# Performance work log

Measured on AMD Instinct MI355X. Metric: run time of the kernel, lower is better.

The kernel has to match this reference:

```python
import jax, jax.numpy as jnp
import numpy as np

B, S, H, KVH, D, HID = 2, 2048, 32, 8, 128, 4096
WINDOW = 512
EPS = 1e-5
SCALE = D ** -0.5
NEG = jnp.finfo(jnp.float32).min


def cohere_layernorm(x, w):
    # true LayerNorm (mean-subtracting), fp32 compute, weight, no bias
    xf = x.astype(jnp.float32)
    mu = jnp.mean(xf, axis=-1, keepdims=True)
    var = jnp.mean((xf - mu) ** 2, axis=-1, keepdims=True)
    return (w.astype(jnp.float32) * (xf - mu) * jax.lax.rsqrt(var + EPS)).astype(x.dtype)


def rotate_half_interleaved(x):
    # interleaved pairs: (x0,x1,x2,x3,...) -> (-x1,x0,-x3,x2,...)
    x1 = x[..., ::2]
    x2 = x[..., 1::2]
    return jnp.stack([-x2, x1], axis=-1).reshape(x.shape)


def setup_inputs() -> dict:
    key = jax.random.key(0)
    ks = jax.random.split(key, 6)
    hidden_states = jax.random.normal(ks[0], (B, S, HID), jnp.float32)
    position_ids = jnp.broadcast_to(jnp.arange(S, dtype=jnp.int32), (B, S))
    # rotary table with interleave-repeated frequencies (Cohere style)
    inv_freq = 1.0 / (10000.0 ** (jnp.arange(0, D, 2, dtype=jnp.float32) / D))
    freqs = jnp.arange(S, dtype=jnp.float32)[:, None] * inv_freq[None, :]  # [S, D/2]
    emb = jnp.repeat(freqs, 2, axis=-1)  # [S, D]
    cos, sin = jnp.cos(emb), jnp.sin(emb)
    std = 0.02
    # weights stored [in, out] so projection is x @ W
    wq = jax.random.normal(ks[1], (HID, H * D), jnp.float32) * std
    wk = jax.random.normal(ks[2], (HID, KVH * D), jnp.float32) * std
    wv = jax.random.normal(ks[3], (HID, KVH * D), jnp.float32) * std
    wo = jax.random.normal(ks[4], (H * D, HID), jnp.float32) * std
    q_norm_w = jnp.ones((D,), jnp.float32)
    k_norm_w = jnp.ones((D,), jnp.float32)
    return {"hidden_states": hidden_states, "position_ids": position_ids,
            "cos": cos, "sin": sin, "wq": wq, "wk": wk, "wv": wv, "wo": wo,
            "q_norm_w": q_norm_w, "k_norm_w": k_norm_w}


def reference(hidden_states, position_ids, cos, sin, wq, wk, wv, wo, q_norm_w, k_norm_w):
    q = (hidden_states @ wq).reshape(B, S, H, D)
    k = (hidden_states @ wk).reshape(B, S, KVH, D)
    v = (hidden_states @ wv).reshape(B, S, KVH, D)
    # QK LayerNorm over head_dim
    q = cohere_layernorm(q, q_norm_w)
    k = cohere_layernorm(k, k_norm_w)
    # interleaved RoPE; cos/sin gathered by position then broadcast over heads (unsqueeze_dim=2)
    c = cos[position_ids][:, :, None, :]  # [B, S, 1, D]
    s = sin[position_ids][:, :, None, :]
    q = q * c + rotate_half_interleaved(q) * s
    k = k * c + rotate_half_interleaved(k) * s
    # GQA: expand KV heads, attention in bhsd layout
    rep = H // KVH
    qh = jnp.transpose(q, (0, 2, 1, 3))                      # [B, H, S, D]
    kh = jnp.transpose(jnp.repeat(k, rep, axis=2), (0, 2, 1, 3))
    vh = jnp.transpose(jnp.repeat(v, rep, axis=2), (0, 2, 1, 3))
    scores = jnp.einsum('bhqd,bhkd->bhqk', qh, kh) * SCALE   # [B, H, S, S]
    i = jnp.arange(S)[:, None]
    j = jnp.arange(S)[None, :]
    mask = (i >= j) & (i - j < WINDOW)                       # causal + sliding window
    scores = jnp.where(mask[None, None], scores, NEG)
    attn = jax.nn.softmax(scores, axis=-1)
    out = jnp.einsum('bhqk,bhkd->bhqd', attn, vh)
    out = jnp.transpose(out, (0, 2, 1, 3)).reshape(B, S, H * D)
    return out @ wo
```

## Files before the change

kernel.cpp:

```cpp
#include <hip/hip_runtime.h>
#include <hip/hip_bf16.h>
#include <cstdio>
#include <cstdint>

#define B_    2
#define S_    2048
#define H_    32
#define KVH_  8
#define D_    128
#define HID_  4096
#define WIN_  512
#define NROW_ (B_*S_)
#define NKV_  2048
#define SCALE_ 0.08838834764831845f
#define SL2E_  0.12751744932973953f

typedef __attribute__((ext_vector_type(8))) __bf16 bf16x8;
typedef __attribute__((ext_vector_type(4))) __bf16 bf16x4;
typedef __attribute__((ext_vector_type(4))) float  f32x4;

#define GAS __attribute__((address_space(1)))
#define LAS __attribute__((address_space(3)))

__global__ __launch_bounds__(256) void cvt_bf16(const float* __restrict__ in,
                                                __hip_bfloat16* __restrict__ out, int n) {
    int i = (blockIdx.x * 256 + threadIdx.x) * 4;
    if (i >= n) return;
    float4 v = *(const float4*)(in + i);
    __hip_bfloat162 a, b;
    a.x = __float2bfloat16(v.x); a.y = __float2bfloat16(v.y);
    b.x = __float2bfloat16(v.z); b.y = __float2bfloat16(v.w);
    *(__hip_bfloat162*)(out + i)     = a;
    *(__hip_bfloat162*)(out + i + 2) = b;
}

__global__ __launch_bounds__(256) void transpose_cvt(const float* __restrict__ in,
                                                     __hip_bfloat16* __restrict__ out,
                                                     int R, int C) {
    __shared__ float t[32][33];
    int tx = threadIdx.x, ty = threadIdx.y;
    int r0 = blockIdx.y * 32, c0 = blockIdx.x * 32;
    #pragma unroll
    for (int i = 0; i < 4; ++i)
        t[ty + 8*i][tx] = in[(size_t)(r0 + ty + 8*i) * C + c0 + tx];
    __syncthreads();
    #pragma unroll
    for (int i = 0; i < 4; ++i)
        out[(size_t)(c0 + ty + 8*i) * R + r0 + tx] = __float2bfloat16(t[tx][ty + 8*i]);
}

__global__ __launch_bounds__(256) void v_transpose(const float* __restrict__ kvf,
                                                   __hip_bfloat16* __restrict__ vt) {
    __shared__ float t[32][33];
    int tx = threadIdx.x, ty = threadIdx.y;
    int plane = blockIdx.z, b = plane >> 3, g = plane & 7;
    int s0 = blockIdx.x * 32, d0 = blockIdx.y * 32;
    #pragma unroll
    for (int i = 0; i < 4; ++i) {
        int s = s0 + ty + 8*i;
        t[ty + 8*i][tx] = kvf[((size_t)b*S_ + s) * NKV_ + (KVH_*D_) + g*D_ + d0 + tx];
    }
    __syncthreads();
    #pragma unroll
    for (int i = 0; i < 4; ++i) {
        int d = d0 + ty + 8*i;
        vt[(((size_t)b*KVH_ + g) * D_ + d) * S_ + s0 + tx] = __float2bfloat16(t[tx][ty + 8*i]);
    }
}

template <int FN>
__global__ __launch_bounds__(512, 2) void gemm_t(const __hip_bfloat16* __restrict__ A,
                                                 const __hip_bfloat16* __restrict__ Bt,
                                                 float* __restrict__ C,
                                                 int M, int N, int K, int nbx) {
    constexpr int BN   = FN * 64;
    constexpr int BLD  = BN / 128;
    constexpr int SLOT = (256 + BN) * 32;
    __shared__ __align__(16) __hip_bfloat16 L[4 * SLOT];
    const int tid  = threadIdx.x;
    const int lane = tid & 63, w = tid >> 6;
    const int wm = w >> 2, wn = w & 3;
    const int lc = lane & 15, lg = lane >> 4;
    const int nwg = gridDim.x, cpx = nwg >> 3;
    const int bid = blockIdx.x;
    const int swz = (bid & 7) * cpx + (bid >> 3);
    const int by = swz / nbx, bx = swz - by * nbx;
    const size_t row0 = (size_t)by * 256, col0 = (size_t)bx * BN;
    const int nt = K >> 5;

    const int srow = tid >> 2;
    const int spc  = tid & 3;
    const int slx  = spc ^ ((srow >> 1) & 3);
    const __hip_bfloat16* Ab = A  + row0 * K;
    const __hip_bfloat16* Bb = Bt + col0 * K;

#define STGA(tile_) do {                                                                   \
    const int ss_ = (tile_) & 3;                                                           \
    const int kt_ = ((tile_) < nt) ? (tile_) : (nt - 1);  \
    _Pragma("unroll")                                                                      \
    for (int rh_ = 0; rh_ < 2; ++rh_)                                                      \
        __builtin_amdgcn_global_load_lds(                                                  \
            (const GAS void*)(Ab + (size_t)(rh_*128 + srow) * K + kt_*32 + slx*8),         \
            (LAS void*)&L[ss_*SLOT + rh_*4096 + w*512], 16, 0, 0);                         \
} while (0)

#define STGB(tile_) do {                                                                   \
    const int ss_ = (tile_) & 3;                                                           \
    const int kt_ = ((tile_) < nt) ? (tile_) : (nt - 1);                                   \
    _Pragma("unroll")                                                                      \
    for (int bh_ = 0; bh_ < BLD; ++bh_)                                                    \
        __builtin_amdgcn_global_load_lds(                                                  \
            (const GAS void*)(Bb + (size_t)(bh_*128 + srow) * K + kt_*32 + slx*8),         \
            (LAS void*)&L[ss_*SLOT + 8192 + bh_*4096 + w*512], 16, 0, 0);                  \
} while (0)

    f32x4 acc[2][4][FN] = {};
    bf16x8 afr[4], bfr[FN];

    STGA(0); STGB(0); STGA(1); STGB(1); STGA(2); STGB(2);
    if constexpr (FN == 4) asm volatile("s_waitcnt vmcnt(8)" ::: "memory");
    else                   asm volatile("s_waitcnt vmcnt(6)" ::: "memory");
    asm volatile("s_barrier" ::: "memory");

    for (int t = 0; t < nt; ++t) {
        const int s_ = t & 3;

        #pragma unroll
        for (int fn = 0; fn < FN; ++fn) {
            const int rB = wn*(FN*16) + fn*16 + lc;
            bfr[fn] = *(const bf16x8*)&L[s_*SLOT + 8192 + rB*32 + ((lg ^ ((rB >> 1) & 3)) * 8)];
        }
        #pragma unroll
        for (int fm = 0; fm < 4; ++fm) {
            const int rA = wm*128 + fm*16 + lc;
            afr[fm] = *(const bf16x8*)&L[s_*SLOT + rA*32 + ((lg ^ ((rA >> 1) & 3)) * 8)];
        }
        STGA(t + 3);
        if constexpr (FN == 4) asm volatile("s_waitcnt vmcnt(10)" ::: "memory");
        else                   asm volatile("s_waitcnt vmcnt(8)"  ::: "memory");
        asm volatile("s_barrier" ::: "memory");
        asm volatile("s_waitcnt lgkmcnt(0)" ::: "memory");
        __builtin_amdgcn_sched_barrier(0);
        __builtin_amdgcn_s_setprio(1);
        #pragma unroll
        for (int fm = 0; fm < 4; ++fm)
            #pragma unroll
            for (int fn = 0; fn < FN; ++fn)
                acc[0][fm][fn] = __builtin_amdgcn_mfma_f32_16x16x32_bf16(
                    afr[fm], bfr[fn], acc[0][fm][fn], 0, 0, 0);
        __builtin_amdgcn_s_setprio(0);

        #pragma unroll
        for (int fm = 0; fm < 4; ++fm) {
            const int rA = wm*128 + 64 + fm*16 + lc;
            afr[fm] = *(const bf16x8*)&L[s_*SLOT + rA*32 + ((lg ^ ((rA >> 1) & 3)) * 8)];
        }
        STGB(t + 3);
        asm volatile("s_waitcnt lgkmcnt(0)" ::: "memory");
        __builtin_amdgcn_sched_barrier(0);
        __builtin_amdgcn_s_setprio(1);
        #pragma unroll
        for (int fm = 0; fm < 4; ++fm)
            #pragma unroll
            for (int fn = 0; fn < FN; ++fn)
                acc[1][fm][fn] = __builtin_amdgcn_mfma_f32_16x16x32_bf16(
                    afr[fm], bfr[fn], acc[1][fm][fn], 0, 0, 0);
        __builtin_amdgcn_s_setprio(0);
        asm volatile("s_barrier" ::: "memory");
    }
#undef STGA
#undef STGB
    asm volatile("s_waitcnt vmcnt(0)" ::: "memory");

    #pragma unroll
    for (int qm = 0; qm < 2; ++qm)
        #pragma unroll
        for (int fm = 0; fm < 4; ++fm)
            #pragma unroll
            for (int fn = 0; fn < FN; ++fn) {
                const size_t col = col0 + wn*(FN*16) + fn*16 + lc;
                #pragma unroll
                for (int rr = 0; rr < 4; ++rr) {
                    const size_t row = row0 + wm*128 + qm*64 + fm*16 + lg*4 + rr;
                    C[row * N + col] = acc[qm][fm][fn][rr];
                }
            }
}

template <int NH, int LD, int XOFF>
__global__ __launch_bounds__(256) void ln_rope(const float* __restrict__ x,
                                               const float* __restrict__ wln,
                                               const float* __restrict__ cosT,
                                               const float* __restrict__ sinT,
                                               const int* __restrict__ pids,
                                               __hip_bfloat16* __restrict__ out) {
    const int lane = threadIdx.x & 63, wv = threadIdx.x >> 6;
    const int r = blockIdx.x * 4 + wv;
    const int h = r % NH;
    const int bs = r / NH;
    const int b = bs / S_, s = bs % S_;
    const float2 xv = *(const float2*)(x + (size_t)bs * LD + XOFF + h*D_ + lane*2);
    float sum = xv.x + xv.y;
    #pragma unroll
    for (int o = 32; o; o >>= 1) sum += __shfl_xor(sum, o);
    const float mu = sum * (1.f / D_);
    const float dx = xv.x - mu, dy = xv.y - mu;
    float vs = dx*dx + dy*dy;
    #pragma unroll
    for (int o = 32; o; o >>= 1) vs += __shfl_xor(vs, o);
    const float rs = rsqrtf(vs * (1.f / D_) + 1e-5f);
    const float2 w2 = *(const float2*)(wln + lane*2);
    const float y0 = w2.x * dx * rs, y1 = w2.y * dy * rs;
    const int p = pids[bs];
    const float2 c  = *(const float2*)(cosT + (size_t)p * D_ + lane*2);
    const float2 sn = *(const float2*)(sinT + (size_t)p * D_ + lane*2);
    __hip_bfloat162 ov;
    ov.x = __float2bfloat16(y0 * c.x - y1 * sn.x);
    ov.y = __float2bfloat16(y1 * c.y + y0 * sn.y);
    *(__hip_bfloat162*)(out + (((size_t)b * NH + h) * S_ + s) * D_ + lane*2) = ov;
}

static __device__ __forceinline__ int sigk_(int r) { return (r & 3) | ((r >> 1) & 4); }

__global__ __launch_bounds__(256) void attn_fwd(const __hip_bfloat16* __restrict__ qr,
                                                const __hip_bfloat16* __restrict__ kr,
                                                const __hip_bfloat16* __restrict__ vt,
                                                __hip_bfloat16* __restrict__ ao) {
    __shared__ __align__(16) __hip_bfloat16 Ksl[2][64*D_];
    __shared__ __align__(16) __hip_bfloat16 Vsl[2][D_*64];
    const int lane = threadIdx.x & 63, w = threadIdx.x >> 6;
    const int lq = lane & 15, lg = lane >> 4;
    const int blk = blockIdx.x;
    const int qt = blk >> 6;
    const int bh = blk & 63;
    const int h = bh & (H_-1), b = bh >> 5;
    const int g = h >> 2;
    const int q0 = qt*64 + w*16;
    const int q  = q0 + lq;

    const __hip_bfloat16* qbase = qr + (((size_t)b*H_ + h)*S_ + q0) * D_;
    const __hip_bfloat16* kbase = kr + ((size_t)b*KVH_ + g) * (size_t)S_ * D_;
    const __hip_bfloat16* vbase = vt + ((size_t)b*KVH_ + g) * (size_t)D_ * S_;

    const int srK = lane >> 4, scK = lane & 15;
    const int srV = lane >> 3, scV = lane & 7;

#define STAGE(nb, k0s) do {                                                              \
    _Pragma("unroll")                                                                    \
    for (int s_ = 0; s_ < 4; ++s_) {                                                     \
        const int rK_ = s_*16 + w*4 + srK;                                               \
        const __hip_bfloat16* srcK_ = kbase + (size_t)((k0s) + rK_)*D_                   \
                                      + ((scK ^ sigk_(rK_)) * 8);                        \
        __builtin_amdgcn_global_load_lds((const GAS void*)srcK_,                         \
            (LAS void*)&Ksl[nb][(s_*16 + w*4)*D_], 16, 0, 0);                            \
    }                                                                                    \
    _Pragma("unroll")                                                                    \
    for (int s_ = 0; s_ < 4; ++s_) {                                                     \
        const int dV_ = s_*32 + w*8 + srV;                                               \
        const __hip_bfloat16* srcV_ = vbase + (size_t)dV_*S_ + (k0s)                     \
                                      + ((scV ^ (dV_ & 7)) * 8);                         \
        __builtin_amdgcn_global_load_lds((const GAS void*)srcV_,                         \
            (LAS void*)&Vsl[nb][(s_*32 + w*8)*64], 16, 0, 0);                            \
    }                                                                                    \
} while (0)

    bf16x8 qf[4];
    #pragma unroll
    for (int kk = 0; kk < 4; ++kk)
        qf[kk] = *(const bf16x8*)(qbase + lq*D_ + kk*32 + lg*8);

    f32x4 o[8] = {};
    float m = -1e30f, l = 0.f;

    int kst = qt*64 - (WIN_ - 1); if (kst < 0) kst = 0; kst &= ~63;
    const int nt = qt + 1 - (kst >> 6);
    const int kldrow = 8*(lq >> 2) + (lq & 3);

    STAGE(0, kst);

    for (int t = 0; t < nt; ++t) {
        const int k0 = kst + t*64;
        const int buf = t & 1;
        if (t + 1 < nt) {
            STAGE((t + 1) & 1, k0 + 64);
            asm volatile("s_waitcnt vmcnt(8)" ::: "memory");
        } else {
            asm volatile("s_waitcnt vmcnt(0)" ::: "memory");
        }
        __builtin_amdgcn_s_barrier();

        f32x4 sc[2][2] = {};
        __builtin_amdgcn_s_setprio(1);
        #pragma unroll
        for (int kb = 0; kb < 2; ++kb)
            #pragma unroll
            for (int f = 0; f < 2; ++f) {
                const int rA = kb*32 + 4*f + kldrow;
                const __hip_bfloat16* kp = &Ksl[buf][rA*D_];
                #pragma unroll
                for (int kk = 0; kk < 4; ++kk) {
                    bf16x8 ka = *(const bf16x8*)(kp + (((kk*4 + lg) ^ sigk_(rA)) * 8));
                    sc[kb][f] = __builtin_amdgcn_mfma_f32_16x16x32_bf16(ka, qf[kk], sc[kb][f], 0, 0, 0);
                }
            }
        __builtin_amdgcn_s_setprio(0);

        const int dqk = q - (k0 + 8*lg);
        float pv[16];
        float mx = -INFINITY;
        #pragma unroll
        for (int kb = 0; kb < 2; ++kb)
            #pragma unroll
            for (int f = 0; f < 2; ++f)
                #pragma unroll
                for (int r = 0; r < 4; ++r) {
                    const int c = kb*32 + 4*f + r;
                    const int d = dqk - c;
                    float v = (d >= 0 && d < WIN_) ? sc[kb][f][r] * SL2E_ : -INFINITY;
                    pv[kb*8 + f*4 + r] = v;
                    mx = fmaxf(mx, v);
                }
        mx = fmaxf(mx, __shfl_xor(mx, 16));
        mx = fmaxf(mx, __shfl_xor(mx, 32));
        const float mn = fmaxf(m, mx);
        const float alpha = exp2f(m - mn);
        float ls = 0.f;
        union { bf16x8 v; __hip_bfloat16 e[8]; } pu[2];
        #pragma unroll
        for (int kb = 0; kb < 2; ++kb)
            #pragma unroll
            for (int j = 0; j < 8; ++j) {
                const float p = exp2f(pv[kb*8 + j] - mn);
                ls += p;
                pu[kb].e[j] = __float2bfloat16(p);
            }
        ls += __shfl_xor(ls, 16);
        ls += __shfl_xor(ls, 32);
        l = l * alpha + ls;
        m = mn;
        #pragma unroll
        for (int n = 0; n < 8; ++n) {
            o[n][0] *= alpha; o[n][1] *= alpha; o[n][2] *= alpha; o[n][3] *= alpha;
        }

        __builtin_amdgcn_s_setprio(1);
        #pragma unroll
        for (int kb = 0; kb < 2; ++kb)
            #pragma unroll
            for (int n = 0; n < 8; ++n) {
                const int dR = n*16 + lq;
                bf16x8 vf8 = *(const bf16x8*)(&Vsl[buf][dR*64] + (((kb*4 + lg) ^ (dR & 7)) * 8));
                o[n] = __builtin_amdgcn_mfma_f32_16x16x32_bf16(vf8, pu[kb].v, o[n], 0, 0, 0);
            }
        __builtin_amdgcn_s_setprio(0);

        if (t + 1 < nt) __builtin_amdgcn_s_barrier();
    }
#undef STAGE

    const float rinv = 1.f / l;
    #pragma unroll
    for (int n = 0; n < 8; ++n) {
        union { bf16x4 v; __hip_bfloat16 e[4]; } ov;
        #pragma unroll
        for (int r = 0; r < 4; ++r) ov.e[r] = __float2bfloat16(o[n][r] * rinv);
        *(bf16x4*)(ao + ((size_t)b*S_ + q)*(H_*D_) + h*D_ + n*16 + lg*4) = ov.v;
    }
}

extern "C" void kernel_launch(void* const* d_in, const int* in_sizes, int n_in,
                              void* d_out, int out_size, void* d_ws, size_t ws_size,
                              hipStream_t stream) {
    const float* hidden = (const float*)d_in[0];
    const int*   pids   = (const int*)  d_in[1];
    const float* cosT   = (const float*)d_in[2];
    const float* sinT   = (const float*)d_in[3];
    const float* wq     = (const float*)d_in[4];
    const float* wk     = (const float*)d_in[5];
    const float* wv     = (const float*)d_in[6];
    const float* wo     = (const float*)d_in[7];
    const float* qnw    = (const float*)d_in[8];
    const float* knw    = (const float*)d_in[9];
    float* out = (float*)d_out;

    char* base = (char*)d_ws;
    size_t off = 0;
    auto take = [&](size_t bytes) -> void* {
        void* q = base + off;
        off = (off + bytes + 255) & ~(size_t)255;
        return q;
    };
    float* qf            = (float*)take((size_t)NROW_*HID_*4);
    float* kvf           = (float*)take((size_t)NROW_*NKV_*4);
    __hip_bfloat16* hb   = (__hip_bfloat16*)take((size_t)NROW_*HID_*2);
    __hip_bfloat16* wqT  = (__hip_bfloat16*)take((size_t)HID_*HID_*2);
    __hip_bfloat16* wkvT = (__hip_bfloat16*)take((size_t)NKV_*HID_*2);
    __hip_bfloat16* woT  = (__hip_bfloat16*)take((size_t)HID_*HID_*2);
    __hip_bfloat16* qr   = (__hip_bfloat16*)take((size_t)B_*H_*S_*D_*2);
    __hip_bfloat16* kr   = (__hip_bfloat16*)take((size_t)B_*KVH_*S_*D_*2);
    __hip_bfloat16* vt   = (__hip_bfloat16*)take((size_t)B_*KVH_*S_*D_*2);
    __hip_bfloat16* ao   = (__hip_bfloat16*)qf;

    if (off > ws_size) {
        fprintf(stderr, "WORKSPACE TOO SMALL: need %zu have %zu\n", off, ws_size);
        return;
    }

    cvt_bf16<<<(NROW_*HID_)/1024, 256, 0, stream>>>(hidden, hb, NROW_*HID_);
    transpose_cvt<<<dim3((H_*D_)/32,   HID_/32), dim3(32,8), 0, stream>>>(wq, wqT, HID_, H_*D_);
    transpose_cvt<<<dim3((KVH_*D_)/32, HID_/32), dim3(32,8), 0, stream>>>(wk, wkvT, HID_, KVH_*D_);
    transpose_cvt<<<dim3((KVH_*D_)/32, HID_/32), dim3(32,8), 0, stream>>>(wv, wkvT + (size_t)(KVH_*D_)*HID_, HID_, KVH_*D_);
    transpose_cvt<<<dim3(HID_/32, (H_*D_)/32),   dim3(32,8), 0, stream>>>(wo, woT, H_*D_, HID_);

    gemm_t<4><<<(NROW_/256)*(HID_/256), 512, 0, stream>>>(hb, wqT,  qf,  NROW_, HID_, HID_, HID_/256);
    gemm_t<2><<<(NROW_/256)*(NKV_/128), 512, 0, stream>>>(hb, wkvT, kvf, NROW_, NKV_, HID_, NKV_/128);

    ln_rope<H_,   HID_, 0><<<(B_*S_*H_)/4,   256, 0, stream>>>(qf,  qnw, cosT, sinT, pids, qr);
    ln_rope<KVH_, NKV_, 0><<<(B_*S_*KVH_)/4, 256, 0, stream>>>(kvf, knw, cosT, sinT, pids, kr);
    v_transpose<<<dim3(S_/32, D_/32, B_*KVH_), dim3(32,8), 0, stream>>>(kvf, vt);

    attn_fwd<<<B_*H_*(S_/64), 256, 0, stream>>>(qr, kr, vt, ao);

    gemm_t<4><<<(NROW_/256)*(HID_/256), 512, 0, stream>>>(ao, woT, out, NROW_, HID_, H_*D_, HID_/256);
}
```

Measured before the change: 513.2 us.

## Fuse V transpose into KV GEMM epilogue, emit bf16 projections, merge weight transposes

```diff
diff --git a/kernel.cpp b/kernel.cpp
--- a/kernel.cpp
+++ b/kernel.cpp
@@ -34,47 +34,40 @@
     *(__hip_bfloat162*)(out + i + 2) = b;
 }
 
-__global__ __launch_bounds__(256) void transpose_cvt(const float* __restrict__ in,
-                                                     __hip_bfloat16* __restrict__ out,
-                                                     int R, int C) {
+__global__ __launch_bounds__(256) void wtrans_all(const float* __restrict__ wq,
+                                                  const float* __restrict__ wk,
+                                                  const float* __restrict__ wv,
+                                                  const float* __restrict__ wo,
+                                                  __hip_bfloat16* __restrict__ wqT,
+                                                  __hip_bfloat16* __restrict__ wkvT,
+                                                  __hip_bfloat16* __restrict__ woT) {
     __shared__ float t[32][33];
-    int tx = threadIdx.x, ty = threadIdx.y;
-    int r0 = blockIdx.y * 32, c0 = blockIdx.x * 32;
+    const int tx = threadIdx.x, ty = threadIdx.y;
+    const int bid = blockIdx.x;
+    const float* src; __hip_bfloat16* dst; int C, idx;
+    if (bid < 16384)      { src = wq; dst = wqT;  C = 4096; idx = bid; }
+    else if (bid < 20480) { src = wk; dst = wkvT; C = 1024; idx = bid - 16384; }
+    else if (bid < 24576) { src = wv; dst = wkvT + (size_t)1024*HID_; C = 1024; idx = bid - 20480; }
+    else                  { src = wo; dst = woT;  C = 4096; idx = bid - 24576; }
+    const int ctiles = C >> 5;
+    const int c0 = (idx % ctiles) * 32, r0 = (idx / ctiles) * 32;
     #pragma unroll
     for (int i = 0; i < 4; ++i)
-        t[ty + 8*i][tx] = in[(size_t)(r0 + ty + 8*i) * C + c0 + tx];
+        t[ty + 8*i][tx] = src[(size_t)(r0 + ty + 8*i) * C + c0 + tx];
     __syncthreads();
     #pragma unroll
     for (int i = 0; i < 4; ++i)
-        out[(size_t)(c0 + ty + 8*i) * R + r0 + tx] = __float2bfloat16(t[tx][ty + 8*i]);
-}
-
-__global__ __launch_bounds__(256) void v_transpose(const float* __restrict__ kvf,
-                                                   __hip_bfloat16* __restrict__ vt) {
-    __shared__ float t[32][33];
-    int tx = threadIdx.x, ty = threadIdx.y;
-    int plane = blockIdx.z, b = plane >> 3, g = plane & 7;
-    int s0 = blockIdx.x * 32, d0 = blockIdx.y * 32;
-    #pragma unroll
-    for (int i = 0; i < 4; ++i) {
-        int s = s0 + ty + 8*i;
-        t[ty + 8*i][tx] = kvf[((size_t)b*S_ + s) * NKV_ + (KVH_*D_) + g*D_ + d0 + tx];
-    }
-    __syncthreads();
-    #pragma unroll
-    for (int i = 0; i < 4; ++i) {
-        int d = d0 + ty + 8*i;
-        vt[(((size_t)b*KVH_ + g) * D_ + d) * S_ + s0 + tx] = __float2bfloat16(t[tx][ty + 8*i]);
-    }
-}
-
-template <int FN>
+        dst[(size_t)(c0 + ty + 8*i) * HID_ + r0 + tx] = __float2bfloat16(t[tx][ty + 8*i]);
+}
+
+template <int FN, int OMODE>
 __global__ __launch_bounds__(512, 2) void gemm_t(const __hip_bfloat16* __restrict__ A,
                                                  const __hip_bfloat16* __restrict__ Bt,
-                                                 float* __restrict__ C,
+                                                 void* __restrict__ Cv, void* __restrict__ C2,
                                                  int M, int N, int K, int nbx) {
     constexpr int BN   = FN * 64;
     constexpr int BLD  = BN / 128;
+    constexpr int LPT  = 2 + BLD;
     constexpr int SLOT = (256 + BN) * 32;
     __shared__ __align__(16) __hip_bfloat16 L[4 * SLOT];
     const int tid  = threadIdx.x;
@@ -114,12 +107,16 @@
             (LAS void*)&L[ss_*SLOT + 8192 + bh_*4096 + w*512], 16, 0, 0);                  \
 } while (0)
 
+#define VMW2L() do {                                                                       \
+    if constexpr (FN == 4) asm volatile("s_waitcnt vmcnt(8)" ::: "memory");                \
+    else                   asm volatile("s_waitcnt vmcnt(6)" ::: "memory");                \
+} while (0)
+
     f32x4 acc[2][4][FN] = {};
     bf16x8 afr[4], bfr[FN];
 
     STGA(0); STGB(0); STGA(1); STGB(1); STGA(2); STGB(2);
-    if constexpr (FN == 4) asm volatile("s_waitcnt vmcnt(8)" ::: "memory");
-    else                   asm volatile("s_waitcnt vmcnt(6)" ::: "memory");
+    VMW2L();
     asm volatile("s_barrier" ::: "memory");
 
     for (int t = 0; t < nt; ++t) {
@@ -136,8 +133,6 @@
             afr[fm] = *(const bf16x8*)&L[s_*SLOT + rA*32 + ((lg ^ ((rA >> 1) & 3)) * 8)];
         }
         STGA(t + 3);
-        if constexpr (FN == 4) asm volatile("s_waitcnt vmcnt(10)" ::: "memory");
-        else                   asm volatile("s_waitcnt vmcnt(8)"  ::: "memory");
         asm volatile("s_barrier" ::: "memory");
         asm volatile("s_waitcnt lgkmcnt(0)" ::: "memory");
         __builtin_amdgcn_sched_barrier(0);
@@ -166,29 +161,92 @@
                 acc[1][fm][fn] = __builtin_amdgcn_mfma_f32_16x16x32_bf16(
                     afr[fm], bfr[fn], acc[1][fm][fn], 0, 0, 0);
         __builtin_amdgcn_s_setprio(0);
+        VMW2L();
         asm volatile("s_barrier" ::: "memory");
     }
 #undef STGA
 #undef STGB
+#undef VMW2L
     asm volatile("s_waitcnt vmcnt(0)" ::: "memory");
 
-    #pragma unroll
-    for (int qm = 0; qm < 2; ++qm)
-        #pragma unroll
-        for (int fm = 0; fm < 4; ++fm)
-            #pragma unroll
-            for (int fn = 0; fn < FN; ++fn) {
-                const size_t col = col0 + wn*(FN*16) + fn*16 + lc;
-                #pragma unroll
-                for (int rr = 0; rr < 4; ++rr) {
-                    const size_t row = row0 + wm*128 + qm*64 + fm*16 + lg*4 + rr;
-                    C[row * N + col] = acc[qm][fm][fn][rr];
+    if constexpr (OMODE == 0) {
+        float* C = (float*)Cv;
+        #pragma unroll
+        for (int qm = 0; qm < 2; ++qm)
+            #pragma unroll
+            for (int fm = 0; fm < 4; ++fm)
+                #pragma unroll
+                for (int fn = 0; fn < FN; ++fn) {
+                    const size_t col = col0 + wn*(FN*16) + fn*16 + lc;
+                    #pragma unroll
+                    for (int rr = 0; rr < 4; ++rr) {
+                        const size_t row = row0 + wm*128 + qm*64 + fm*16 + lg*4 + rr;
+                        C[row * N + col] = acc[qm][fm][fn][rr];
+                    }
                 }
+    } else if constexpr (OMODE == 1) {
+        __hip_bfloat16* C = (__hip_bfloat16*)Cv;
+        #pragma unroll
+        for (int qm = 0; qm < 2; ++qm)
+            #pragma unroll
+            for (int fm = 0; fm < 4; ++fm)
+                #pragma unroll
+                for (int fn = 0; fn < FN; ++fn) {
+                    const size_t col = col0 + wn*(FN*16) + fn*16 + lc;
+                    #pragma unroll
+                    for (int rr = 0; rr < 4; ++rr) {
+                        const size_t row = row0 + wm*128 + qm*64 + fm*16 + lg*4 + rr;
+                        C[row * N + col] = __float2bfloat16(acc[qm][fm][fn][rr]);
+                    }
+                }
+    } else {
+        if (bx < 8) {
+            __hip_bfloat16* C = (__hip_bfloat16*)Cv;
+            #pragma unroll
+            for (int qm = 0; qm < 2; ++qm)
+                #pragma unroll
+                for (int fm = 0; fm < 4; ++fm)
+                    #pragma unroll
+                    for (int fn = 0; fn < FN; ++fn) {
+                        const size_t col = col0 + wn*32 + fn*16 + lc;
+                        #pragma unroll
+                        for (int rr = 0; rr < 4; ++rr) {
+                            const size_t row = row0 + wm*128 + qm*64 + fm*16 + lg*4 + rr;
+                            C[row * 1024 + col] = __float2bfloat16(acc[qm][fm][fn][rr]);
+                        }
+                    }
+        } else {
+            __hip_bfloat16* lt = (__hip_bfloat16*)L;
+            __syncthreads();
+            #pragma unroll
+            for (int qm = 0; qm < 2; ++qm)
+                #pragma unroll
+                for (int fm = 0; fm < 4; ++fm)
+                    #pragma unroll
+                    for (int fn = 0; fn < FN; ++fn) {
+                        const int cl = wn*32 + fn*16 + lc;
+                        #pragma unroll
+                        for (int rr = 0; rr < 4; ++rr) {
+                            const int rl = wm*128 + qm*64 + fm*16 + lg*4 + rr;
+                            lt[cl*264 + rl] = __float2bfloat16(acc[qm][fm][fn][rr]);
+                        }
+                    }
+            __syncthreads();
+            const int bb = (int)(row0 >> 11), s0 = (int)(row0 & 2047);
+            const int g  = (int)((col0 - 1024) >> 7);
+            __hip_bfloat16* vto = (__hip_bfloat16*)C2 + (((size_t)bb*KVH_ + g) * D_) * (size_t)S_;
+            const int d = tid >> 2, sc0 = (tid & 3) * 64;
+            #pragma unroll
+            for (int j = 0; j < 64; j += 8) {
+                bf16x8 v = *(const bf16x8*)&lt[d*264 + sc0 + j];
+                *(bf16x8*)&vto[(size_t)d*S_ + s0 + sc0 + j] = v;
             }
+        }
+    }
 }
 
 template <int NH, int LD, int XOFF>
-__global__ __launch_bounds__(256) void ln_rope(const float* __restrict__ x,
+__global__ __launch_bounds__(256) void ln_rope(const __hip_bfloat16* __restrict__ x,
                                                const float* __restrict__ wln,
                                                const float* __restrict__ cosT,
                                                const float* __restrict__ sinT,
@@ -199,12 +257,13 @@
     const int h = r % NH;
     const int bs = r / NH;
     const int b = bs / S_, s = bs % S_;
-    const float2 xv = *(const float2*)(x + (size_t)bs * LD + XOFF + h*D_ + lane*2);
-    float sum = xv.x + xv.y;
+    const __hip_bfloat162 xv2 = *(const __hip_bfloat162*)(x + (size_t)bs * LD + XOFF + h*D_ + lane*2);
+    const float x0 = __bfloat162float(xv2.x), x1 = __bfloat162float(xv2.y);
+    float sum = x0 + x1;
     #pragma unroll
     for (int o = 32; o; o >>= 1) sum += __shfl_xor(sum, o);
     const float mu = sum * (1.f / D_);
-    const float dx = xv.x - mu, dy = xv.y - mu;
+    const float dx = x0 - mu, dy = x1 - mu;
     float vs = dx*dx + dy*dy;
     #pragma unroll
     for (int o = 32; o; o >>= 1) vs += __shfl_xor(vs, o);
@@ -390,8 +449,8 @@
         off = (off + bytes + 255) & ~(size_t)255;
         return q;
     };
-    float* qf            = (float*)take((size_t)NROW_*HID_*4);
-    float* kvf           = (float*)take((size_t)NROW_*NKV_*4);
+    __hip_bfloat16* qfb  = (__hip_bfloat16*)take((size_t)NROW_*HID_*2);
+    __hip_bfloat16* kf   = (__hip_bfloat16*)take((size_t)NROW_*1024*2);
     __hip_bfloat16* hb   = (__hip_bfloat16*)take((size_t)NROW_*HID_*2);
     __hip_bfloat16* wqT  = (__hip_bfloat16*)take((size_t)HID_*HID_*2);
     __hip_bfloat16* wkvT = (__hip_bfloat16*)take((size_t)NKV_*HID_*2);
@@ -399,7 +458,7 @@
     __hip_bfloat16* qr   = (__hip_bfloat16*)take((size_t)B_*H_*S_*D_*2);
     __hip_bfloat16* kr   = (__hip_bfloat16*)take((size_t)B_*KVH_*S_*D_*2);
     __hip_bfloat16* vt   = (__hip_bfloat16*)take((size_t)B_*KVH_*S_*D_*2);
-    __hip_bfloat16* ao   = (__hip_bfloat16*)qf;
+    __hip_bfloat16* ao   = qfb;
 
     if (off > ws_size) {
         fprintf(stderr, "WORKSPACE TOO SMALL: need %zu have %zu\n", off, ws_size);
@@ -407,19 +466,15 @@
     }
 
     cvt_bf16<<<(NROW_*HID_)/1024, 256, 0, stream>>>(hidden, hb, NROW_*HID_);
-    transpose_cvt<<<dim3((H_*D_)/32,   HID_/32), dim3(32,8), 0, stream>>>(wq, wqT, HID_, H_*D_);
-    transpose_cvt<<<dim3((KVH_*D_)/32, HID_/32), dim3(32,8), 0, stream>>>(wk, wkvT, HID_, KVH_*D_);
-    transpose_cvt<<<dim3((KVH_*D_)/32, HID_/32), dim3(32,8), 0, stream>>>(wv, wkvT + (size_t)(KVH_*D_)*HID_, HID_, KVH_*D_);
-    transpose_cvt<<<dim3(HID_/32, (H_*D_)/32),   dim3(32,8), 0, stream>>>(wo, woT, H_*D_, HID_);
-
-    gemm_t<4><<<(NROW_/256)*(HID_/256), 512, 0, stream>>>(hb, wqT,  qf,  NROW_, HID_, HID_, HID_/256);
-    gemm_t<2><<<(NROW_/256)*(NKV_/128), 512, 0, stream>>>(hb, wkvT, kvf, NROW_, NKV_, HID_, NKV_/128);
-
-    ln_rope<H_,   HID_, 0><<<(B_*S_*H_)/4,   256, 0, stream>>>(qf,  qnw, cosT, sinT, pids, qr);
-    ln_rope<KVH_, NKV_, 0><<<(B_*S_*KVH_)/4, 256, 0, stream>>>(kvf, knw, cosT, sinT, pids, kr);
-    v_transpose<<<dim3(S_/32, D_/32, B_*KVH_), dim3(32,8), 0, stream>>>(kvf, vt);
+    wtrans_all<<<40960, dim3(32,8), 0, stream>>>(wq, wk, wv, wo, wqT, wkvT, woT);
+
+    gemm_t<4,1><<<(NROW_/256)*(HID_/256), 512, 0, stream>>>(hb, wqT,  qfb, nullptr, NROW_, HID_, HID_, HID_/256);
+    gemm_t<2,2><<<(NROW_/256)*(NKV_/128), 512, 0, stream>>>(hb, wkvT, kf,  vt,      NROW_, NKV_, HID_, NKV_/128);
+
+    ln_rope<H_,   HID_, 0><<<(B_*S_*H_)/4,   256, 0, stream>>>(qfb, qnw, cosT, sinT, pids, qr);
+    ln_rope<KVH_, 1024, 0><<<(B_*S_*KVH_)/4, 256, 0, stream>>>(kf,  knw, cosT, sinT, pids, kr);
 
     attn_fwd<<<B_*H_*(S_/64), 256, 0, stream>>>(qr, kr, vt, ao);
 
-    gemm_t<4><<<(NROW_/256)*(HID_/256), 512, 0, stream>>>(ao, woT, out, NROW_, HID_, H_*D_, HID_/256);
-}
+    gemm_t<4,0><<<(NROW_/256)*(HID_/256), 512, 0, stream>>>(ao, woT, out, nullptr, NROW_, HID_, H_*D_, HID_/256);
+}
```

Result: faster. 490.3 us (-4.5%).
